# Kernel optimization log

Measured on AMD Instinct MI355X. Metric: run time of the kernel, lower is better.

Reference implementation:

```python
import jax, jax.numpy as jnp
import numpy as np

KS = 5          # dilated_kernel_size
LIM = KS // 2   # positions live in [-2, 2]
B = 2048


def _construct_kernel(w, p1, p2):
    """DCLS v1ste kernel construction.
    w, p1, p2: (Cout, Cin, kernel_count) -> dense kernel (Cout, Cin, KS, KS).
    Forward: each element's weight is scattered to the NEAREST integer grid
    position (straight-through rounding of the bilinear fractional parts).
    """
    q1 = p1 + LIM
    q2 = p2 + LIM
    i1 = jnp.floor(q1)
    i2 = jnp.floor(q2)
    r1 = q1 - i1
    r2 = q2 - i2
    # straight-through estimator: forward = hard round, backward = identity
    r1 = jax.lax.stop_gradient(jnp.where(r1 >= 0.5, 1.0, 0.0) - r1) + r1
    r2 = jax.lax.stop_gradient(jnp.where(r2 >= 0.5, 1.0, 0.0) - r2) + r2
    i1 = i1.astype(jnp.int32)
    i2 = i2.astype(jnp.int32)
    # one_hot of out-of-range index is all-zero, which drops invalid neighbors
    a = (1.0 - r1)[..., None] * jax.nn.one_hot(i1, KS) + r1[..., None] * jax.nn.one_hot(i1 + 1, KS)
    b = (1.0 - r2)[..., None] * jax.nn.one_hot(i2, KS) + r2[..., None] * jax.nn.one_hot(i2 + 1, KS)
    return jnp.einsum('oik,oika,oikb->oiab', w, a, b)


def _conv(x, k, pad):
    return jax.lax.conv_general_dilated(x, k, (1, 1), [(pad, pad), (pad, pad)])


def _maxpool2(x):
    return jax.lax.reduce_window(x, -jnp.inf, jax.lax.max, (1, 1, 2, 2), (1, 1, 2, 2), 'VALID')


def setup_inputs() -> dict:
    key = jax.random.key(0)
    ks = jax.random.split(key, 12)
    x = jax.random.normal(ks[0], (B, 1, 28, 28), dtype=jnp.float32)
    w1 = jax.random.normal(ks[1], (32, 1, 26), dtype=jnp.float32) * 0.2
    p1 = jax.random.uniform(ks[2], (32, 1, 26), minval=-LIM, maxval=LIM, dtype=jnp.float32)
    p2 = jax.random.uniform(ks[3], (32, 1, 26), minval=-LIM, maxval=LIM, dtype=jnp.float32)
    b1 = jnp.zeros((32,), dtype=jnp.float32)
    w2 = jax.random.normal(ks[4], (64, 32, 3, 3), dtype=jnp.float32) * 0.06
    b2 = jnp.zeros((64,), dtype=jnp.float32)
    fc1_w = jax.random.normal(ks[5], (128, 64 * 14 * 14), dtype=jnp.float32) * 0.009
    fc1_b = jnp.zeros((128,), dtype=jnp.float32)
    fc2_w = jax.random.normal(ks[6], (10, 128), dtype=jnp.float32) * 0.09
    fc2_b = jnp.zeros((10,), dtype=jnp.float32)
    return {"x": x, "w1": w1, "p1": p1, "p2": p2, "b1": b1, "w2": w2,
            "b2": b2, "fc1_w": fc1_w, "fc1_b": fc1_b, "fc2_w": fc2_w, "fc2_b": fc2_b}


def reference(x, w1, p1, p2, b1, w2, b2, fc1_w, fc1_b, fc2_w, fc2_b):
    k1 = _construct_kernel(w1, p1, p2)                      # (32,1,5,5)
    h = jax.nn.relu(_conv(x, k1, 2) + b1[None, :, None, None])   # (B,32,28,28)
    h = jax.nn.relu(_conv(h, w2, 1) + b2[None, :, None, None])   # (B,64,28,28)
    h = _maxpool2(h)                                        # (B,64,14,14)
    h = h.reshape(-1, 64 * 14 * 14)
    h = jax.nn.relu(h @ fc1_w.T + fc1_b)
    return h @ fc2_w.T + fc2_b
```

## Files before the change

kernel.cpp:

```cpp
#include <hip/hip_runtime.h>
#include <hip/hip_bf16.h>

typedef __attribute__((ext_vector_type(8))) short bf16x8;
typedef __attribute__((ext_vector_type(4))) float f32x4;
typedef __attribute__((ext_vector_type(4))) unsigned int u32x4;
typedef __attribute__((ext_vector_type(2))) unsigned int u32x2;

#define NB 2048

static __device__ __forceinline__ unsigned short f2bf(float f) {
  unsigned int u = __builtin_bit_cast(unsigned int, f);
  u += 0x7fffu + ((u >> 16) & 1u);
  return (unsigned short)(u >> 16);
}
static __device__ __forceinline__ unsigned int cvtpk(float lo, float hi) {
  unsigned int r;
  asm("v_cvt_pk_bf16_f32 %0, %1, %2" : "=v"(r) : "v"(lo), "v"(hi));
  return r;
}

__global__ __launch_bounds__(256) void k_prep(
    const float* __restrict__ w2, const float* __restrict__ fc1w,
    const float* __restrict__ w1, const float* __restrict__ p1,
    const float* __restrict__ p2,
    unsigned short* __restrict__ w2b, unsigned short* __restrict__ fc1wb,
    unsigned short* __restrict__ k1b) {
  const int gid = blockIdx.x * blockDim.x + threadIdx.x;
  if (gid < 401408) {
    const int j0 = gid * 4;
    const int kw = j0 & 31;
    const int n  = (j0 >> 5) & 127;
    const int q  = j0 >> 12;
    f32x4 v = *(const f32x4*)&fc1w[n*12544 + q*32 + kw];
    u32x2 r = { cvtpk(v[0], v[1]), cvtpk(v[2], v[3]) };
    *(u32x2*)&fc1wb[j0] = r;
  } else if (gid < 401408 + 18432) {
    int i = gid - 401408;
    int cin = i & 31;
    int cout = (i >> 5) & 63;
    int kk = i >> 11;
    int ky = kk / 3, kx = kk % 3;
    w2b[i] = f2bf(w2[((cout*32 + cin)*3 + ky)*3 + kx]);
  } else if (gid < 401408 + 18432 + 1024) {
    int t = gid - (401408 + 18432);
    int o = t >> 5, tap = t & 31;
    unsigned short r = 0;
    if (tap < 25) {
      int a = tap / 5, bcol = tap % 5;
      float acc = 0.f;
      for (int k = 0; k < 26; ++k) {
        float q1 = p1[o*26 + k] + 2.0f;
        float q2 = p2[o*26 + k] + 2.0f;
        float f1 = floorf(q1), f2 = floorf(q2);
        int idx1 = (int)f1 + ((q1 - f1) >= 0.5f ? 1 : 0);
        int idx2 = (int)f2 + ((q2 - f2) >= 0.5f ? 1 : 0);
        if (idx1 == a && idx2 == bcol) acc += w1[o*26 + k];
      }
      r = f2bf(acc);
    }
    k1b[t] = r;
  }
}

__global__ __launch_bounds__(256, 3) void k_conv(
    const float* __restrict__ x, const unsigned short* __restrict__ k1b,
    const float* __restrict__ b1, const unsigned short* __restrict__ w2b,
    const float* __restrict__ b2, unsigned short* __restrict__ h3) {
  __shared__ __align__(16) float xs[32*36];
  __shared__ __align__(16) unsigned short h1s[16*32*32];

  const int t = threadIdx.x;
  const int bimg = blockIdx.x;
  const int lane = t & 63;
  const int wid = t >> 6;
  const int l15 = lane & 15;
  const int lk = lane >> 4;

  for (int i = t; i < 1152; i += 256) {
    int iy = i / 36, ix = i - iy*36;
    float v = 0.f;
    if (iy >= 2 && iy < 30 && ix >= 2 && ix < 30)
      v = x[bimg*784 + (iy-2)*28 + (ix-2)];
    xs[i] = v;
  }

  int off[8];
  #pragma unroll
  for (int j = 0; j < 8; ++j) {
    int tp = lk*8 + j; tp = tp > 24 ? 24 : tp;
    int ky = tp / 5;
    off[j] = ky*36 + (tp - ky*5);
  }
  const bf16x8 k1a0 = *(const bf16x8*)&k1b[l15*32 + lk*8];
  const bf16x8 k1a1 = *(const bf16x8*)&k1b[(16 + l15)*32 + lk*8];
  f32x4 b1i0, b1i1;
  #pragma unroll
  for (int r = 0; r < 4; ++r) {
    b1i0[r] = b1[lk*4 + r];
    b1i1[r] = b1[16 + lk*4 + r];
  }

  const int ntp = wid & 1;
  const int tx  = wid >> 1;
  bf16x8 bfr[2][9];
  #pragma unroll
  for (int nn = 0; nn < 2; ++nn)
    #pragma unroll
    for (int kk = 0; kk < 9; ++kk)
      bfr[nn][kk] = *(const bf16x8*)&w2b[(kk*64 + (ntp*2+nn)*16 + l15)*32 + lk*8];
  f32x4 b2i[2];
  #pragma unroll
  for (int nn = 0; nn < 2; ++nn) {
    float bb = b2[ntp*32 + nn*16 + l15];
    b2i[nn] = (f32x4){bb, bb, bb, bb};
  }
  int colOff[3];
  #pragma unroll
  for (int kx = 0; kx < 3; ++kx) {
    int xk = tx*16 + l15 + kx; xk = xk > 31 ? 31 : xk;
    colOff[kx] = xk*64 + ((lk ^ ((xk >> 1) & 3)) << 4);
  }

  const int mtile = bimg >> 4, mi = bimg & 15;
  unsigned short* h3m = h3 + (size_t)mtile*200704 + mi*32;

  __syncthreads();

  for (int half = 0; half < 2; ++half) {
    if (half) __syncthreads();

    {
      u32x4* H = (u32x4*)h1s;
      u32x4 z = {0u,0u,0u,0u};
      const int zrow = half ? 15 : 0;
      if (t < 128) H[zrow*128 + t] = z;
      const int r0 = half ? 0 : 1;
      if (t < 240) {
        int rr = t >> 4, rem = t & 15;
        int pi = rem >> 2, sub = rem & 3;
        int px = pi == 0 ? 0 : 28 + pi;
        H[((r0 + rr)*32 + px)*4 + sub] = z;
      }
    }

    const int ybase = half ? 13 : 0;
    for (int tid = wid; tid < 30; tid += 4) {
      const int ty = tid >> 1;
      const int x0 = (tid & 1) << 4;
      const int yo = ybase + ty;
      const float* bp = &xs[yo*36 + x0 + l15];
      u32x4 bw;
      bw[0] = cvtpk(bp[off[0]], bp[off[1]]);
      bw[1] = cvtpk(bp[off[2]], bp[off[3]]);
      bw[2] = cvtpk(bp[off[4]], bp[off[5]]);
      bw[3] = cvtpk(bp[off[6]], bp[off[7]]);
      const bf16x8 bfrag = __builtin_bit_cast(bf16x8, bw);
      f32x4 d0 = b1i0, d1 = b1i1;
      d0 = __builtin_amdgcn_mfma_f32_16x16x32_bf16(k1a0, bfrag, d0, 0, 0, 0);
      d1 = __builtin_amdgcn_mfma_f32_16x16x32_bf16(k1a1, bfrag, d1, 0, 0, 0);
      const int xo = x0 + l15;
      if (xo < 28) {
        const int ry = half ? (yo - 13) : (yo + 1);
        const int pix = ry*32 + xo + 1;
        const int swz = (pix >> 1) & 3;
        const int blkbase = (lk >> 1);
        unsigned int w0lo = cvtpk(fmaxf(d0[0], 0.f), fmaxf(d0[1], 0.f));
        unsigned int w0hi = cvtpk(fmaxf(d0[2], 0.f), fmaxf(d0[3], 0.f));
        unsigned int w1lo = cvtpk(fmaxf(d1[0], 0.f), fmaxf(d1[1], 0.f));
        unsigned int w1hi = cvtpk(fmaxf(d1[2], 0.f), fmaxf(d1[3], 0.f));
        char* base = (char*)h1s + pix*64 + (lk & 1)*8;
        *(u32x2*)(base + ((blkbase ^ swz) << 4))       = (u32x2){w0lo, w0hi};
        *(u32x2*)(base + (((2 + blkbase) ^ swz) << 4)) = (u32x2){w1lo, w1hi};
      }
    }
    __syncthreads();

    const char* h1c = (const char*)h1s;
    for (int pyl = 0; pyl < 7; ++pyl) {
      const int py = half*7 + pyl;
      const int rbase = (2*py - (half ? 14 : 0)) * 2048;
      f32x4 acc[2][2];
      #pragma unroll
      for (int yi = 0; yi < 2; ++yi)
        #pragma unroll
        for (int nn = 0; nn < 2; ++nn) acc[yi][nn] = b2i[nn];
      #pragma unroll
      for (int kx = 0; kx < 3; ++kx) {
        bf16x8 af[4];
        #pragma unroll
        for (int r = 0; r < 4; ++r)
          af[r] = *(const bf16x8*)(h1c + rbase + r*2048 + colOff[kx]);
        #pragma unroll
        for (int ky = 0; ky < 3; ++ky)
          #pragma unroll
          for (int yi = 0; yi < 2; ++yi) {
            acc[yi][0] = __builtin_amdgcn_mfma_f32_16x16x32_bf16(af[yi+ky], bfr[0][ky*3+kx], acc[yi][0], 0, 0, 0);
            acc[yi][1] = __builtin_amdgcn_mfma_f32_16x16x32_bf16(af[yi+ky], bfr[1][ky*3+kx], acc[yi][1], 0, 0, 0);
          }
      }
      float hm[2][2][2];
      #pragma unroll
      for (int yi = 0; yi < 2; ++yi)
        #pragma unroll
        for (int nn = 0; nn < 2; ++nn) {
          float v0 = fmaxf(acc[yi][nn][0], 0.f);
          float v1 = fmaxf(acc[yi][nn][1], 0.f);
          float v2 = fmaxf(acc[yi][nn][2], 0.f);
          float v3 = fmaxf(acc[yi][nn][3], 0.f);
          hm[nn][yi][0] = fmaxf(v0, v1);
          hm[nn][yi][1] = fmaxf(v2, v3);
        }
      if (!(tx == 1 && lk == 3)) {
        const int px0 = tx*8 + lk*2;
        #pragma unroll
        for (int nn = 0; nn < 2; ++nn) {
          float q0 = fmaxf(hm[nn][0][0], hm[nn][1][0]);
          float q1 = fmaxf(hm[nn][0][1], hm[nn][1][1]);
          const int c = ntp*32 + nn*16 + l15;
          const int k0 = c*196 + py*14 + px0;
          *(unsigned int*)&h3m[(k0 >> 5)*512 + (k0 & 31)] = cvtpk(q0, q1);
        }
      }
    }
  }
}

__global__ __launch_bounds__(256) void k_fc1(const unsigned short* __restrict__ h3,
                                             const unsigned short* __restrict__ fc1wb,
                                             float* __restrict__ h4p) {
  const int bid = blockIdx.x;
  const int mtile = bid >> 3, kh = bid & 7;
  const int t = threadIdx.x, lane = t & 63, w = t >> 6;
  const int l15 = lane & 15, lk = lane >> 4;
  const int lo = l15*32 + lk*8;

  const unsigned short* ap  = h3    + (size_t)mtile*200704 + (size_t)(kh*49)*512 + lo;
  const unsigned short* b0p = fc1wb + (size_t)(kh*49)*4096 + (w*32)*32 + lo;

  f32x4 acc0 = {0.f,0.f,0.f,0.f}, acc1 = {0.f,0.f,0.f,0.f};
  #pragma unroll 7
  for (int ks = 0; ks < 49; ++ks) {
    bf16x8 a  = *(const bf16x8*)(ap  + ks*512);
    bf16x8 w0 = *(const bf16x8*)(b0p + ks*4096);
    bf16x8 w1 = *(const bf16x8*)(b0p + ks*4096 + 512);
    acc0 = __builtin_amdgcn_mfma_f32_16x16x32_bf16(a, w0, acc0, 0, 0, 0);
    acc1 = __builtin_amdgcn_mfma_f32_16x16x32_bf16(a, w1, acc1, 0, 0, 0);
  }
  float* outp = h4p + (size_t)kh * NB * 128;
  const int n0 = w*32 + l15;
  #pragma unroll
  for (int jj = 0; jj < 4; ++jj) {
    const int bb = mtile*16 + lk*4 + jj;
    outp[bb*128 + n0]      = acc0[jj];
    outp[bb*128 + n0 + 16] = acc1[jj];
  }
}

__global__ __launch_bounds__(256) void k_fc2(const float* __restrict__ h4p,
                                             const float* __restrict__ fc1b,
                                             const float* __restrict__ fc2w,
                                             const float* __restrict__ fc2b,
                                             float* __restrict__ out) {
  __shared__ float hs[8*129];
  const int blk = blockIdx.x;
  const int t = threadIdx.x;
  for (int i = t; i < 1024; i += 256) {
    const int base = blk*1024 + i;
    float v = 0.f;
    #pragma unroll
    for (int kh = 0; kh < 8; ++kh) v += h4p[base + kh*262144];
    v += fc1b[i & 127];
    hs[(i >> 7)*129 + (i & 127)] = fmaxf(v, 0.f);
  }
  __syncthreads();
  if (t < 80) {
    const int bb = t / 10, n = t - (t/10)*10;
    float acc = fc2b[n];
    const float* wr = fc2w + n*128;
    const float* hr = hs + bb*129;
    #pragma unroll 8
    for (int k = 0; k < 128; ++k) acc = fmaf(hr[k], wr[k], acc);
    out[(blk*8 + bb)*10 + n] = acc;
  }
}

extern "C" void kernel_launch(void* const* d_in, const int* in_sizes, int n_in,
                              void* d_out, int out_size, void* d_ws, size_t ws_size,
                              hipStream_t stream) {
  const float* x    = (const float*)d_in[0];
  const float* w1   = (const float*)d_in[1];
  const float* p1   = (const float*)d_in[2];
  const float* p2   = (const float*)d_in[3];
  const float* b1   = (const float*)d_in[4];
  const float* w2   = (const float*)d_in[5];
  const float* b2   = (const float*)d_in[6];
  const float* fc1w = (const float*)d_in[7];
  const float* fc1b = (const float*)d_in[8];
  const float* fc2w = (const float*)d_in[9];
  const float* fc2b = (const float*)d_in[10];

  if (ws_size < 63021056u) return;
  char* ws = (char*)d_ws;
  unsigned short* k1b  = (unsigned short*)(ws + 0);
  unsigned short* w2b  = (unsigned short*)(ws + 4096);
  unsigned short* fc1wb= (unsigned short*)(ws + 40960);
  unsigned short* h3   = (unsigned short*)(ws + 3252224);
  float* h4p           = (float*)(ws + 54632448);

  k_prep<<<(401408 + 18432 + 1024 + 255) / 256, 256, 0, stream>>>(
      w2, fc1w, w1, p1, p2, w2b, fc1wb, k1b);
  k_conv<<<NB, 256, 0, stream>>>(x, k1b, b1, w2b, b2, h3);
  k_fc1<<<1024, 256, 0, stream>>>(h3, fc1wb, h4p);
  k_fc2<<<256, 256, 0, stream>>>(h4p, fc1b, fc2w, fc2b, (float*)d_out);
}
```

Before: 116.4 us.

## Register-block fc1 over two batch tiles and remap conv block-to-image order

The fc1 kernel now computes two 16-row batch tiles per block, so each loaded fc1 weight fragment feeds four MFMAs instead of two. This halves the grid and redundant weight traffic, at the cost of more accumulator registers and fewer blocks. The conv kernel remaps blockIdx to images so consecutive blocks are spread across the batch, presumably to improve locality or distribution across XCDs. The rbase expression is also simplified to an equivalent form.

```diff
diff --git a/kernel.cpp b/kernel.cpp
--- a/kernel.cpp
+++ b/kernel.cpp
@@ -70,7 +70,7 @@
   __shared__ __align__(16) unsigned short h1s[16*32*32];
 
   const int t = threadIdx.x;
-  const int bimg = blockIdx.x;
+  const int bimg = (blockIdx.x & 7) * 256 + (blockIdx.x >> 3);
   const int lane = t & 63;
   const int wid = t >> 6;
   const int l15 = lane & 15;
@@ -178,7 +178,7 @@
     const char* h1c = (const char*)h1s;
     for (int pyl = 0; pyl < 7; ++pyl) {
       const int py = half*7 + pyl;
-      const int rbase = (2*py - (half ? 14 : 0)) * 2048;
+      const int rbase = pyl*2*2048;
       f32x4 acc[2][2];
       #pragma unroll
       for (int yi = 0; yi < 2; ++yi)
@@ -225,34 +225,41 @@
   }
 }
 
-__global__ __launch_bounds__(256) void k_fc1(const unsigned short* __restrict__ h3,
-                                             const unsigned short* __restrict__ fc1wb,
-                                             float* __restrict__ h4p) {
+__global__ __launch_bounds__(256, 2) void k_fc1(const unsigned short* __restrict__ h3,
+                                                const unsigned short* __restrict__ fc1wb,
+                                                float* __restrict__ h4p) {
   const int bid = blockIdx.x;
-  const int mtile = bid >> 3, kh = bid & 7;
+  const int m2 = bid >> 3, kh = bid & 7;
   const int t = threadIdx.x, lane = t & 63, w = t >> 6;
   const int l15 = lane & 15, lk = lane >> 4;
   const int lo = l15*32 + lk*8;
 
-  const unsigned short* ap  = h3    + (size_t)mtile*200704 + (size_t)(kh*49)*512 + lo;
+  const unsigned short* a0p = h3 + (size_t)(2*m2)*200704 + (size_t)(kh*49)*512 + lo;
+  const unsigned short* a1p = a0p + 200704;
   const unsigned short* b0p = fc1wb + (size_t)(kh*49)*4096 + (w*32)*32 + lo;
 
-  f32x4 acc0 = {0.f,0.f,0.f,0.f}, acc1 = {0.f,0.f,0.f,0.f};
+  f32x4 acc00 = {0.f,0.f,0.f,0.f}, acc01 = {0.f,0.f,0.f,0.f};
+  f32x4 acc10 = {0.f,0.f,0.f,0.f}, acc11 = {0.f,0.f,0.f,0.f};
   #pragma unroll 7
   for (int ks = 0; ks < 49; ++ks) {
-    bf16x8 a  = *(const bf16x8*)(ap  + ks*512);
+    bf16x8 a0 = *(const bf16x8*)(a0p + ks*512);
+    bf16x8 a1 = *(const bf16x8*)(a1p + ks*512);
     bf16x8 w0 = *(const bf16x8*)(b0p + ks*4096);
     bf16x8 w1 = *(const bf16x8*)(b0p + ks*4096 + 512);
-    acc0 = __builtin_amdgcn_mfma_f32_16x16x32_bf16(a, w0, acc0, 0, 0, 0);
-    acc1 = __builtin_amdgcn_mfma_f32_16x16x32_bf16(a, w1, acc1, 0, 0, 0);
+    acc00 = __builtin_amdgcn_mfma_f32_16x16x32_bf16(a0, w0, acc00, 0, 0, 0);
+    acc01 = __builtin_amdgcn_mfma_f32_16x16x32_bf16(a0, w1, acc01, 0, 0, 0);
+    acc10 = __builtin_amdgcn_mfma_f32_16x16x32_bf16(a1, w0, acc10, 0, 0, 0);
+    acc11 = __builtin_amdgcn_mfma_f32_16x16x32_bf16(a1, w1, acc11, 0, 0, 0);
   }
   float* outp = h4p + (size_t)kh * NB * 128;
   const int n0 = w*32 + l15;
+  const int bb0 = m2*32 + lk*4;
   #pragma unroll
   for (int jj = 0; jj < 4; ++jj) {
-    const int bb = mtile*16 + lk*4 + jj;
-    outp[bb*128 + n0]      = acc0[jj];
-    outp[bb*128 + n0 + 16] = acc1[jj];
+    outp[(bb0 + jj)*128 + n0]           = acc00[jj];
+    outp[(bb0 + jj)*128 + n0 + 16]      = acc01[jj];
+    outp[(bb0 + 16 + jj)*128 + n0]      = acc10[jj];
+    outp[(bb0 + 16 + jj)*128 + n0 + 16] = acc11[jj];
   }
 }
 
@@ -310,6 +317,6 @@
   k_prep<<<(401408 + 18432 + 1024 + 255) / 256, 256, 0, stream>>>(
       w2, fc1w, w1, p1, p2, w2b, fc1wb, k1b);
   k_conv<<<NB, 256, 0, stream>>>(x, k1b, b1, w2b, b2, h3);
-  k_fc1<<<1024, 256, 0, stream>>>(h3, fc1wb, h4p);
+  k_fc1<<<512, 256, 0, stream>>>(h3, fc1wb, h4p);
   k_fc2<<<256, 256, 0, stream>>>(h4p, fc1b, fc2w, fc2b, (float*)d_out);
 }
```

Result: faster. 111.9 us (-3.9%).
